# Kernel tuning notes

Hardware: AMD Instinct MI355X
Metric: run time of the kernel (lower is better)

## Reference

```python
import jax, jax.numpy as jnp
import numpy as np

EPS = 1e-6          # VNLinearLeakyReLU eps
NEG_SLOPE = 0.2     # leaky relu slope
K = 16              # k-NN neighbors
F_EPS = 1e-12       # F.normalize eps


def vn_linear_leaky(x, Wf, Wd):
    # x: [B, Cin, 3, ...]; Wf, Wd: [Cout, Cin] (torch nn.Linear, no bias)
    p = jnp.einsum('oc,bc...->bo...', Wf, x)
    d = jnp.einsum('oc,bc...->bo...', Wd, x)
    dot = jnp.sum(p * d, axis=2, keepdims=True)
    d_sq = jnp.sum(d * d, axis=2, keepdims=True)
    mask = (dot >= 0).astype(x.dtype)
    return NEG_SLOPE * p + (1.0 - NEG_SLOPE) * (
        mask * p + (1.0 - mask) * (p - (dot / (d_sq + EPS)) * d))


def channel_equi_vec_normalize(x):
    # x: [B, C, 3, ...]
    norm = jnp.linalg.norm(x, axis=2, keepdims=True)            # [B,C,1,...]
    x_dir = x / jnp.maximum(norm, F_EPS)                        # F.normalize(dim=2)
    ch_norm = jnp.linalg.norm(norm, axis=1, keepdims=True)      # [B,1,1,...]
    x_nn = norm / jnp.maximum(ch_norm, F_EPS)                   # F.normalize(dim=1)
    return x_dir * x_nn


def get_graph_feature(y, k):
    # y: [B, C, 3, N] -> [B, 2C, 3, N, k]  (DGCNN/VN graph feature)
    B, C, _, N = y.shape
    yf = y.reshape(B, C * 3, N)
    sq = jnp.sum(yf * yf, axis=1)                               # [B,N]
    inner = jnp.einsum('bcn,bcm->bnm', yf, yf)
    neg_dist = 2.0 * inner - sq[:, :, None] - sq[:, None, :]    # -||yi-yj||^2
    _, idx = jax.lax.top_k(neg_dist, k)                         # [B,N,k] int32
    yp = jnp.transpose(y, (0, 3, 1, 2))                         # [B,N,C,3]
    nbr = jax.vmap(lambda pts, ids: pts[ids])(yp, idx)          # [B,N,k,C,3]
    center = jnp.broadcast_to(yp[:, :, None], nbr.shape)        # [B,N,k,C,3]
    feat = jnp.concatenate([nbr - center, center], axis=3)      # [B,N,k,2C,3]
    return jnp.transpose(feat, (0, 3, 4, 1, 2))                 # [B,2C,3,N,k]


def setup_inputs() -> dict:
    key = jax.random.key(0)
    ks = jax.random.split(key, 8)
    B, C, N = 2, 32, 768
    x = jax.random.normal(ks[0], (B, C, 3, N), dtype=jnp.float32)
    y = jax.random.normal(ks[1], (B, C, 3, N), dtype=jnp.float32)
    def lin(k, o, i):
        return jax.random.normal(k, (o, i), dtype=jnp.float32) / jnp.sqrt(jnp.float32(i))
    return {
        'x': x, 'y': y,
        'Wq_f': lin(ks[2], 32, 32), 'Wq_d': lin(ks[3], 32, 32),
        'Wk_f': lin(ks[4], 32, 64), 'Wk_d': lin(ks[5], 32, 64),
        'Wv_f': lin(ks[6], 32, 64), 'Wv_d': lin(ks[7], 32, 64),
    }


def reference(x, y, Wq_f, Wq_d, Wk_f, Wk_d, Wv_f, Wv_d):
    Qx = channel_equi_vec_normalize(vn_linear_leaky(x, Wq_f, Wq_d))   # [B,32,3,N]
    g = get_graph_feature(y, K)                                       # [B,64,3,N,K]
    Ky = channel_equi_vec_normalize(vn_linear_leaky(g, Wk_f, Wk_d))   # [B,32,3,N,K]
    Vy = vn_linear_leaky(g, Wv_f, Wv_d)                               # [B,32,3,N,K]
    # Original: Qx repeated over k, matmul([N,k],[k,N]) -> attn[n,m] = Qx[n]*sum_j Ky[m,j]
    scale = 1.0 / jnp.sqrt(jnp.float32(3 * 32))
    Ksum = jnp.sum(Ky, axis=-1)                                       # [B,32,3,N]
    attn = Qx[..., :, None] * Ksum[..., None, :] * scale              # [B,32,3,N,N]
    ax = jax.nn.softmax(attn, axis=-1)
    # sum_k(ax @ Vy) == ax @ sum_k(Vy)
    Vsum = jnp.sum(Vy, axis=-1)                                       # [B,32,3,N]
    out = jnp.einsum('bcdnm,bcdm->bcdn', ax, Vsum)
    return x + out
```

## Files before the change

### kernel.cpp

```cpp
#include <hip/hip_runtime.h>

#define NPTS 768
#define SCALE 0.10206207261596575f

static __device__ const float CFACT[13] = {
  1.0f, 1.0f, 0.5f, 0.16666667f, 0.041666668f, 0.008333334f, 0.0013888889f,
  1.9841270e-4f, 2.4801587e-5f, 2.7557319e-6f, 2.7557319e-7f, 2.5052108e-8f, 2.0876757e-9f
};

__global__ __launch_bounds__(256) void ka_pre(const float* __restrict__ x,
    const float* __restrict__ y,
    const float* __restrict__ Wqf, const float* __restrict__ Wqd,
    const float* __restrict__ Wkf, const float* __restrict__ Wkd,
    const float* __restrict__ Wvf, const float* __restrict__ Wvd,
    float* __restrict__ qx, float* __restrict__ Pb, float* __restrict__ Rb,
    int* __restrict__ idxout)
{
  __shared__ __align__(16) char smem[34816];
  int tid = threadIdx.x;
  if (blockIdx.x < 192) {
    float2* w2 = (float2*)smem;
    float4 (*xs)[32] = (float4(*)[32])(smem + 8192);
    for (int i = tid; i < 1024; i += 256) {
      int cin = i >> 5, c = i & 31;
      w2[i] = make_float2(Wqf[c * 32 + cin], Wqd[c * 32 + cin]);
    }
    int g = tid >> 5, c = tid & 31;
    int p = blockIdx.x * 8 + g;
    int b = p / NPTS, n = p % NPTS;
    for (int t = c; t < 96; t += 32) {
      float v = x[(b * 96 + t) * NPTS + n];
      ((float*)&xs[g][t / 3])[t % 3] = v;
    }
    __syncthreads();
    float pf0 = 0, pf1 = 0, pf2 = 0, pd0 = 0, pd1 = 0, pd2 = 0;
#pragma unroll
    for (int cin = 0; cin < 32; cin++) {
      float2 w = w2[(cin << 5) + c];
      float4 xv = xs[g][cin];
      pf0 = fmaf(w.x, xv.x, pf0); pf1 = fmaf(w.x, xv.y, pf1); pf2 = fmaf(w.x, xv.z, pf2);
      pd0 = fmaf(w.y, xv.x, pd0); pd1 = fmaf(w.y, xv.y, pd1); pd2 = fmaf(w.y, xv.z, pd2);
    }
    float dot = pf0 * pd0 + pf1 * pd1 + pf2 * pd2;
    float dsq = pd0 * pd0 + pd1 * pd1 + pd2 * pd2;
    float q0 = pf0, q1 = pf1, q2 = pf2;
    if (dot < 0.f) {
      float r = 0.8f * dot / (dsq + 1e-6f);
      q0 -= r * pd0; q1 -= r * pd1; q2 -= r * pd2;
    }
    float nrm = sqrtf(q0 * q0 + q1 * q1 + q2 * q2);
    float n2 = nrm * nrm;
#pragma unroll
    for (int m = 1; m <= 16; m <<= 1) n2 += __shfl_xor(n2, m);
    float fac = (nrm / fmaxf(sqrtf(n2), 1e-12f)) / fmaxf(nrm, 1e-12f);
    int base = ((b * 32 + c) * 3) * NPTS + n;
    qx[base] = q0 * fac; qx[base + NPTS] = q1 * fac; qx[base + 2 * NPTS] = q2 * fac;
  } else if (blockIdx.x < 576) {
    float4* wLs = (float4*)smem;
    float4* wDs = (float4*)(smem + 16384);
    float4 (*xs)[32] = (float4(*)[32])(smem + 32768);
    for (int i = tid; i < 1024; i += 256) {
      int cin = i >> 5, c = i & 31;
      float kfL = Wkf[c * 64 + cin], kdL = Wkd[c * 64 + cin];
      float vfL = Wvf[c * 64 + cin], vdL = Wvd[c * 64 + cin];
      wLs[i] = make_float4(kfL, kdL, vfL, vdL);
      wDs[i] = make_float4(Wkf[c * 64 + 32 + cin] - kfL, Wkd[c * 64 + 32 + cin] - kdL,
                           Wvf[c * 64 + 32 + cin] - vfL, Wvd[c * 64 + 32 + cin] - vdL);
    }
    int g = tid >> 6, lane = tid & 63, half = lane >> 5, c = lane & 31;
    int p = (blockIdx.x - 192) * 4 + g;
    int b = p / NPTS, n = p % NPTS;
    for (int t = lane; t < 96; t += 64) {
      float v = y[(b * 96 + t) * NPTS + n];
      ((float*)&xs[g][t / 3])[t % 3] = v;
    }
    __syncthreads();
    const float4* wsel = half ? wDs : wLs;
    float kf0 = 0, kf1 = 0, kf2 = 0, kd0 = 0, kd1 = 0, kd2 = 0;
    float vf0 = 0, vf1 = 0, vf2 = 0, vd0 = 0, vd1 = 0, vd2 = 0;
#pragma unroll 8
    for (int cin = 0; cin < 32; cin++) {
      float4 wv = wsel[(cin << 5) + c];
      float4 xv = xs[g][cin];
      kf0 = fmaf(wv.x, xv.x, kf0); kf1 = fmaf(wv.x, xv.y, kf1); kf2 = fmaf(wv.x, xv.z, kf2);
      kd0 = fmaf(wv.y, xv.x, kd0); kd1 = fmaf(wv.y, xv.y, kd1); kd2 = fmaf(wv.y, xv.z, kd2);
      vf0 = fmaf(wv.z, xv.x, vf0); vf1 = fmaf(wv.z, xv.y, vf1); vf2 = fmaf(wv.z, xv.z, vf2);
      vd0 = fmaf(wv.w, xv.x, vd0); vd1 = fmaf(wv.w, xv.y, vd1); vd2 = fmaf(wv.w, xv.z, vd2);
    }
    float* dst = half ? Rb : Pb;
    size_t base = ((size_t)(b * NPTS + n) * 32 + c) * 12;
    float4* Dp = (float4*)(dst + base);
    Dp[0] = make_float4(kf0, kf1, kf2, kd0);
    Dp[1] = make_float4(kd1, kd2, vf0, vf1);
    Dp[2] = make_float4(vf2, vd0, vd1, vd2);
  } else {
    float4 (*as4)[24] = (float4(*)[24])smem;
    unsigned int (*kd)[NPTS] = (unsigned int(*)[NPTS])(smem + 1536);
    int kb = blockIdx.x - 576;
    int b = kb / 192;
    int n0 = (kb % 192) * 4;
    const float* yb = y + b * 96 * NPTS;
    for (int i = tid; i < 384; i += 256) {
      int j = i / 96, f = i % 96;
      ((float*)as4)[j * 96 + f] = yb[f * NPTS + n0 + j];
    }
    __syncthreads();
    float in[12];
    float sqm[3] = {0.f, 0.f, 0.f};
#pragma unroll
    for (int t = 0; t < 12; t++) in[t] = 0.f;
#pragma unroll 4
    for (int f4 = 0; f4 < 24; f4++) {
      float4 a0 = as4[0][f4], a1 = as4[1][f4], a2 = as4[2][f4], a3 = as4[3][f4];
#pragma unroll
      for (int r = 0; r < 3; r++) {
        int m = r * 256 + tid;
        const float* col = yb + (f4 * 4) * NPTS + m;
        float b0 = col[0], b1 = col[NPTS], b2 = col[2 * NPTS], b3 = col[3 * NPTS];
        sqm[r] = fmaf(b0, b0, fmaf(b1, b1, fmaf(b2, b2, fmaf(b3, b3, sqm[r]))));
        in[0 + r] = fmaf(a0.x, b0, fmaf(a0.y, b1, fmaf(a0.z, b2, fmaf(a0.w, b3, in[0 + r]))));
        in[3 + r] = fmaf(a1.x, b0, fmaf(a1.y, b1, fmaf(a1.z, b2, fmaf(a1.w, b3, in[3 + r]))));
        in[6 + r] = fmaf(a2.x, b0, fmaf(a2.y, b1, fmaf(a2.z, b2, fmaf(a2.w, b3, in[6 + r]))));
        in[9 + r] = fmaf(a3.x, b0, fmaf(a3.y, b1, fmaf(a3.z, b2, fmaf(a3.w, b3, in[9 + r]))));
      }
    }
#pragma unroll
    for (int j = 0; j < 4; j++) {
#pragma unroll
      for (int r = 0; r < 3; r++) {
        int m = r * 256 + tid;
        float v = 2.f * in[j * 3 + r] - sqm[r];
        unsigned int u = __float_as_uint(v);
        u = (u & 0x80000000u) ? ~u : (u | 0x80000000u);
        kd[j][m] = u;
      }
    }
    __syncthreads();
    int w = tid >> 6, lane = tid & 63;
    unsigned long long kk[12];
#pragma unroll
    for (int j = 0; j < 12; j++) {
      int m = lane + 64 * j;
      kk[j] = ((unsigned long long)kd[w][m] << 10) | (unsigned)(1023 - m);
    }
    int outbase = (b * NPTS + n0 + w) * 16;
    for (int it = 0; it < 16; it++) {
      unsigned long long a0 = kk[0] > kk[1] ? kk[0] : kk[1];
      unsigned long long a1 = kk[2] > kk[3] ? kk[2] : kk[3];
      unsigned long long a2 = kk[4] > kk[5] ? kk[4] : kk[5];
      unsigned long long a3 = kk[6] > kk[7] ? kk[6] : kk[7];
      unsigned long long a4 = kk[8] > kk[9] ? kk[8] : kk[9];
      unsigned long long a5 = kk[10] > kk[11] ? kk[10] : kk[11];
      unsigned long long b0 = a0 > a1 ? a0 : a1;
      unsigned long long b1 = a2 > a3 ? a2 : a3;
      unsigned long long b2 = a4 > a5 ? a4 : a5;
      unsigned long long best = b0 > b1 ? b0 : b1;
      best = best > b2 ? best : b2;
#pragma unroll
      for (int off = 1; off <= 32; off <<= 1) {
        unsigned long long o = __shfl_xor(best, off);
        best = o > best ? o : best;
      }
      int wm = 1023 - (int)(best & 1023u);
      if (lane == 0) idxout[outbase + it] = wm;
      int jj = wm >> 6;
      bool me = (lane == (wm & 63));
      switch (jj) {
        case 0:  kk[0]  = me ? 0ull : kk[0];  break;
        case 1:  kk[1]  = me ? 0ull : kk[1];  break;
        case 2:  kk[2]  = me ? 0ull : kk[2];  break;
        case 3:  kk[3]  = me ? 0ull : kk[3];  break;
        case 4:  kk[4]  = me ? 0ull : kk[4];  break;
        case 5:  kk[5]  = me ? 0ull : kk[5];  break;
        case 6:  kk[6]  = me ? 0ull : kk[6];  break;
        case 7:  kk[7]  = me ? 0ull : kk[7];  break;
        case 8:  kk[8]  = me ? 0ull : kk[8];  break;
        case 9:  kk[9]  = me ? 0ull : kk[9];  break;
        case 10: kk[10] = me ? 0ull : kk[10]; break;
        default: kk[11] = me ? 0ull : kk[11]; break;
      }
    }
  }
}

__global__ __launch_bounds__(256) void kb_kv(const float* __restrict__ Pb,
    const float* __restrict__ Rb, const int* __restrict__ idxw,
    float* __restrict__ ksum, float* __restrict__ vsum)
{
  __shared__ float red[2][6][32];
  int tid = threadIdx.x;
  int w = tid >> 6;
  int pt = w >> 1;
  int wh = w & 1;
  int lane = tid & 63, kh = lane >> 5, c = lane & 31;
  int p = blockIdx.x * 2 + pt;
  int b = p / NPTS, n = p % NPTS;
  const float4* Rp = (const float4*)(Rb + ((size_t)(b * NPTS + n) * 32 + c) * 12);
  float4 r0 = Rp[0], r1 = Rp[1], r2 = Rp[2];
  int ibase = (b * NPTS + n) * 16 + wh * 8 + kh * 4;
  int4 ia = *(const int4*)(idxw + ibase);
  int ms[4] = {ia.x, ia.y, ia.z, ia.w};
  float ks0 = 0, ks1 = 0, ks2 = 0, vs0 = 0, vs1 = 0, vs2 = 0;
#pragma unroll
  for (int j = 0; j < 4; j++) {
    const float4* Pp = (const float4*)(Pb + ((size_t)(b * NPTS + ms[j]) * 32 + c) * 12);
    float4 p0 = Pp[0], p1 = Pp[1], p2 = Pp[2];
    float kf0 = p0.x + r0.x, kf1 = p0.y + r0.y, kf2 = p0.z + r0.z;
    float kd0 = p0.w + r0.w, kd1 = p1.x + r1.x, kd2 = p1.y + r1.y;
    float vf0 = p1.z + r1.z, vf1 = p1.w + r1.w, vf2 = p2.x + r2.x;
    float vd0 = p2.y + r2.y, vd1 = p2.z + r2.z, vd2 = p2.w + r2.w;
    float dot = kf0 * kd0 + kf1 * kd1 + kf2 * kd2;
    float dsq = kd0 * kd0 + kd1 * kd1 + kd2 * kd2;
    float k0 = kf0, k1 = kf1, k2 = kf2;
    if (dot < 0.f) { float r = 0.8f * dot / (dsq + 1e-6f); k0 -= r * kd0; k1 -= r * kd1; k2 -= r * kd2; }
    float nrm = sqrtf(k0 * k0 + k1 * k1 + k2 * k2);
    float n2 = nrm * nrm;
#pragma unroll
    for (int mm = 1; mm <= 16; mm <<= 1) n2 += __shfl_xor(n2, mm);
    float fac = (nrm / fmaxf(sqrtf(n2), 1e-12f)) / fmaxf(nrm, 1e-12f);
    ks0 = fmaf(k0, fac, ks0); ks1 = fmaf(k1, fac, ks1); ks2 = fmaf(k2, fac, ks2);
    float dotv = vf0 * vd0 + vf1 * vd1 + vf2 * vd2;
    float dsqv = vd0 * vd0 + vd1 * vd1 + vd2 * vd2;
    float v0 = vf0, v1 = vf1, v2 = vf2;
    if (dotv < 0.f) { float r = 0.8f * dotv / (dsqv + 1e-6f); v0 -= r * vd0; v1 -= r * vd1; v2 -= r * vd2; }
    vs0 += v0; vs1 += v1; vs2 += v2;
  }
  ks0 += __shfl_xor(ks0, 32); ks1 += __shfl_xor(ks1, 32); ks2 += __shfl_xor(ks2, 32);
  vs0 += __shfl_xor(vs0, 32); vs1 += __shfl_xor(vs1, 32); vs2 += __shfl_xor(vs2, 32);
  if (kh == 0 && wh == 1) {
    red[pt][0][c] = ks0; red[pt][1][c] = ks1; red[pt][2][c] = ks2;
    red[pt][3][c] = vs0; red[pt][4][c] = vs1; red[pt][5][c] = vs2;
  }
  __syncthreads();
  if (kh == 0 && wh == 0) {
    ks0 += red[pt][0][c]; ks1 += red[pt][1][c]; ks2 += red[pt][2][c];
    vs0 += red[pt][3][c]; vs1 += red[pt][4][c]; vs2 += red[pt][5][c];
    int base = ((b * 32 + c) * 3) * NPTS + n;
    ksum[base] = ks0 * SCALE; ksum[base + NPTS] = ks1 * SCALE; ksum[base + 2 * NPTS] = ks2 * SCALE;
    vsum[base] = vs0; vsum[base + NPTS] = vs1; vsum[base + 2 * NPTS] = vs2;
  }
}

__global__ __launch_bounds__(256) void kc_attn(const float* __restrict__ x,
    const float* __restrict__ qx, const float* __restrict__ ks, const float* __restrict__ vs,
    float* __restrict__ out)
{
  __shared__ float red[4][25];
  __shared__ float AB[26];
  int tid = threadIdx.x;
  int sl = blockIdx.x;
  const float* srow = ks + sl * NPTS;
  const float* vrow = vs + sl * NPTS;
  float P[12], Q[13];
#pragma unroll
  for (int t = 0; t < 12; t++) P[t] = 0.f;
#pragma unroll
  for (int t = 0; t < 13; t++) Q[t] = 0.f;
  for (int m = tid; m < NPTS; m += 256) {
    float s = srow[m], v = vrow[m];
    Q[0] += v;
    float pw = s;
#pragma unroll
    for (int t = 0; t < 12; t++) {
      P[t] += pw;
      Q[t + 1] = fmaf(pw, v, Q[t + 1]);
      pw *= s;
    }
  }
#pragma unroll
  for (int off = 1; off <= 32; off <<= 1) {
#pragma unroll
    for (int t = 0; t < 12; t++) P[t] += __shfl_xor(P[t], off);
#pragma unroll
    for (int t = 0; t < 13; t++) Q[t] += __shfl_xor(Q[t], off);
  }
  int lane = tid & 63, wid = tid >> 6;
  if (lane == 0) {
#pragma unroll
    for (int t = 0; t < 12; t++) red[wid][t] = P[t];
#pragma unroll
    for (int t = 0; t < 13; t++) red[wid][12 + t] = Q[t];
  }
  __syncthreads();
  if (tid < 25) {
    float sm = red[0][tid] + red[1][tid] + red[2][tid] + red[3][tid];
    if (tid < 12) AB[1 + tid] = CFACT[1 + tid] * sm;
    else          AB[13 + (tid - 12)] = CFACT[tid - 12] * sm;
  }
  if (tid == 25) AB[0] = (float)NPTS;
  __syncthreads();
#pragma unroll
  for (int nn = 0; nn < 3; nn++) {
    int n = nn * 256 + tid;
    float q = qx[sl * NPTS + n];
    float den = AB[12], num = AB[25];
#pragma unroll
    for (int t = 11; t >= 0; t--) {
      den = fmaf(den, q, AB[t]);
      num = fmaf(num, q, AB[13 + t]);
    }
    out[sl * NPTS + n] = x[sl * NPTS + n] + num / den;
  }
}

extern "C" void kernel_launch(void* const* d_in, const int* in_sizes, int n_in,
                              void* d_out, int out_size, void* d_ws, size_t ws_size,
                              hipStream_t stream) {
  const float* x   = (const float*)d_in[0];
  const float* y   = (const float*)d_in[1];
  const float* Wqf = (const float*)d_in[2];
  const float* Wqd = (const float*)d_in[3];
  const float* Wkf = (const float*)d_in[4];
  const float* Wkd = (const float*)d_in[5];
  const float* Wvf = (const float*)d_in[6];
  const float* Wvd = (const float*)d_in[7];
  float* out = (float*)d_out;

  float* qx   = (float*)d_ws;
  float* ksum = qx + 147456;
  float* vsum = ksum + 147456;
  int*   idx  = (int*)(vsum + 147456);
  float* Pb   = (float*)(idx + 24576);
  float* Rb   = Pb + 589824;

  ka_pre <<<960, 256, 0, stream>>>(x, y, Wqf, Wqd, Wkf, Wkd, Wvf, Wvd, qx, Pb, Rb, idx);
  kb_kv  <<<768, 256, 0, stream>>>(Pb, Rb, idx, ksum, vsum);
  kc_attn<<<192, 256, 0, stream>>>(x, qx, ksum, vsum, out);
}
```

Before: 114.5 us.

## Merge Q projection into KV blocks and widen kNN tiles to eight rows

The Q-projection branch is folded into the K/V projection blocks, so each block loads both x and y for its point and the lower half of each wave also computes the normalized Qx. The kNN branch now handles 8 query rows per block instead of 4, which halves the number of times each y column is reread from global memory. Each wave then runs the top-16 selection for two rows in sequence. Grid size drops from 960 to 576 blocks, at the cost of more shared memory, more registers in the distance loop, and longer serial top-k work per block.

New measurement: 123.4 us. 7.7% more time.

```diff
diff --git a/kernel.cpp b/kernel.cpp
--- a/kernel.cpp
+++ b/kernel.cpp
@@ -16,49 +16,14 @@
     float* __restrict__ qx, float* __restrict__ Pb, float* __restrict__ Rb,
     int* __restrict__ idxout)
 {
-  __shared__ __align__(16) char smem[34816];
+  __shared__ __align__(16) char smem[45056];
   int tid = threadIdx.x;
-  if (blockIdx.x < 192) {
-    float2* w2 = (float2*)smem;
-    float4 (*xs)[32] = (float4(*)[32])(smem + 8192);
-    for (int i = tid; i < 1024; i += 256) {
-      int cin = i >> 5, c = i & 31;
-      w2[i] = make_float2(Wqf[c * 32 + cin], Wqd[c * 32 + cin]);
-    }
-    int g = tid >> 5, c = tid & 31;
-    int p = blockIdx.x * 8 + g;
-    int b = p / NPTS, n = p % NPTS;
-    for (int t = c; t < 96; t += 32) {
-      float v = x[(b * 96 + t) * NPTS + n];
-      ((float*)&xs[g][t / 3])[t % 3] = v;
-    }
-    __syncthreads();
-    float pf0 = 0, pf1 = 0, pf2 = 0, pd0 = 0, pd1 = 0, pd2 = 0;
-#pragma unroll
-    for (int cin = 0; cin < 32; cin++) {
-      float2 w = w2[(cin << 5) + c];
-      float4 xv = xs[g][cin];
-      pf0 = fmaf(w.x, xv.x, pf0); pf1 = fmaf(w.x, xv.y, pf1); pf2 = fmaf(w.x, xv.z, pf2);
-      pd0 = fmaf(w.y, xv.x, pd0); pd1 = fmaf(w.y, xv.y, pd1); pd2 = fmaf(w.y, xv.z, pd2);
-    }
-    float dot = pf0 * pd0 + pf1 * pd1 + pf2 * pd2;
-    float dsq = pd0 * pd0 + pd1 * pd1 + pd2 * pd2;
-    float q0 = pf0, q1 = pf1, q2 = pf2;
-    if (dot < 0.f) {
-      float r = 0.8f * dot / (dsq + 1e-6f);
-      q0 -= r * pd0; q1 -= r * pd1; q2 -= r * pd2;
-    }
-    float nrm = sqrtf(q0 * q0 + q1 * q1 + q2 * q2);
-    float n2 = nrm * nrm;
-#pragma unroll
-    for (int m = 1; m <= 16; m <<= 1) n2 += __shfl_xor(n2, m);
-    float fac = (nrm / fmaxf(sqrtf(n2), 1e-12f)) / fmaxf(nrm, 1e-12f);
-    int base = ((b * 32 + c) * 3) * NPTS + n;
-    qx[base] = q0 * fac; qx[base + NPTS] = q1 * fac; qx[base + 2 * NPTS] = q2 * fac;
-  } else if (blockIdx.x < 576) {
+  if (blockIdx.x < 384) {
     float4* wLs = (float4*)smem;
     float4* wDs = (float4*)(smem + 16384);
-    float4 (*xs)[32] = (float4(*)[32])(smem + 32768);
+    float2* wq2 = (float2*)(smem + 32768);
+    float4 (*xs)[32] = (float4(*)[32])(smem + 40960);
+    float4 (*xq)[32] = (float4(*)[32])(smem + 43008);
     for (int i = tid; i < 1024; i += 256) {
       int cin = i >> 5, c = i & 31;
       float kfL = Wkf[c * 64 + cin], kdL = Wkd[c * 64 + cin];
@@ -66,13 +31,14 @@
       wLs[i] = make_float4(kfL, kdL, vfL, vdL);
       wDs[i] = make_float4(Wkf[c * 64 + 32 + cin] - kfL, Wkd[c * 64 + 32 + cin] - kdL,
                            Wvf[c * 64 + 32 + cin] - vfL, Wvd[c * 64 + 32 + cin] - vdL);
+      wq2[i] = make_float2(Wqf[c * 32 + cin], Wqd[c * 32 + cin]);
     }
     int g = tid >> 6, lane = tid & 63, half = lane >> 5, c = lane & 31;
-    int p = (blockIdx.x - 192) * 4 + g;
+    int p = blockIdx.x * 4 + g;
     int b = p / NPTS, n = p % NPTS;
     for (int t = lane; t < 96; t += 64) {
-      float v = y[(b * 96 + t) * NPTS + n];
-      ((float*)&xs[g][t / 3])[t % 3] = v;
+      ((float*)&xs[g][t / 3])[t % 3] = y[(b * 96 + t) * NPTS + n];
+      ((float*)&xq[g][t / 3])[t % 3] = x[(b * 96 + t) * NPTS + n];
     }
     __syncthreads();
     const float4* wsel = half ? wDs : wLs;
@@ -93,39 +59,68 @@
     Dp[0] = make_float4(kf0, kf1, kf2, kd0);
     Dp[1] = make_float4(kd1, kd2, vf0, vf1);
     Dp[2] = make_float4(vf2, vd0, vd1, vd2);
+    if (half == 0) {
+      float pf0 = 0, pf1 = 0, pf2 = 0, pd0 = 0, pd1 = 0, pd2 = 0;
+#pragma unroll 8
+      for (int cin = 0; cin < 32; cin++) {
+        float2 w = wq2[(cin << 5) + c];
+        float4 xv = xq[g][cin];
+        pf0 = fmaf(w.x, xv.x, pf0); pf1 = fmaf(w.x, xv.y, pf1); pf2 = fmaf(w.x, xv.z, pf2);
+        pd0 = fmaf(w.y, xv.x, pd0); pd1 = fmaf(w.y, xv.y, pd1); pd2 = fmaf(w.y, xv.z, pd2);
+      }
+      float dot = pf0 * pd0 + pf1 * pd1 + pf2 * pd2;
+      float dsq = pd0 * pd0 + pd1 * pd1 + pd2 * pd2;
+      float q0 = pf0, q1 = pf1, q2 = pf2;
+      if (dot < 0.f) {
+        float r = 0.8f * dot / (dsq + 1e-6f);
+        q0 -= r * pd0; q1 -= r * pd1; q2 -= r * pd2;
+      }
+      float nrm = sqrtf(q0 * q0 + q1 * q1 + q2 * q2);
+      float n2 = nrm * nrm;
+#pragma unroll
+      for (int m = 1; m <= 16; m <<= 1) n2 += __shfl_xor(n2, m);
+      float fac = (nrm / fmaxf(sqrtf(n2), 1e-12f)) / fmaxf(nrm, 1e-12f);
+      int qb = ((b * 32 + c) * 3) * NPTS + n;
+      qx[qb] = q0 * fac; qx[qb + NPTS] = q1 * fac; qx[qb + 2 * NPTS] = q2 * fac;
+    }
   } else {
     float4 (*as4)[24] = (float4(*)[24])smem;
-    unsigned int (*kd)[NPTS] = (unsigned int(*)[NPTS])(smem + 1536);
-    int kb = blockIdx.x - 576;
-    int b = kb / 192;
-    int n0 = (kb % 192) * 4;
+    unsigned int (*kd)[NPTS] = (unsigned int(*)[NPTS])(smem + 3072);
+    int kbn = blockIdx.x - 384;
+    int b = kbn / 96;
+    int n0 = (kbn % 96) * 8;
     const float* yb = y + b * 96 * NPTS;
-    for (int i = tid; i < 384; i += 256) {
+    for (int i = tid; i < 768; i += 256) {
       int j = i / 96, f = i % 96;
       ((float*)as4)[j * 96 + f] = yb[f * NPTS + n0 + j];
     }
     __syncthreads();
-    float in[12];
+    float in[24];
     float sqm[3] = {0.f, 0.f, 0.f};
 #pragma unroll
-    for (int t = 0; t < 12; t++) in[t] = 0.f;
-#pragma unroll 4
+    for (int t = 0; t < 24; t++) in[t] = 0.f;
+#pragma unroll 2
     for (int f4 = 0; f4 < 24; f4++) {
       float4 a0 = as4[0][f4], a1 = as4[1][f4], a2 = as4[2][f4], a3 = as4[3][f4];
+      float4 a4 = as4[4][f4], a5 = as4[5][f4], a6 = as4[6][f4], a7 = as4[7][f4];
 #pragma unroll
       for (int r = 0; r < 3; r++) {
         int m = r * 256 + tid;
         const float* col = yb + (f4 * 4) * NPTS + m;
         float b0 = col[0], b1 = col[NPTS], b2 = col[2 * NPTS], b3 = col[3 * NPTS];
         sqm[r] = fmaf(b0, b0, fmaf(b1, b1, fmaf(b2, b2, fmaf(b3, b3, sqm[r]))));
-        in[0 + r] = fmaf(a0.x, b0, fmaf(a0.y, b1, fmaf(a0.z, b2, fmaf(a0.w, b3, in[0 + r]))));
-        in[3 + r] = fmaf(a1.x, b0, fmaf(a1.y, b1, fmaf(a1.z, b2, fmaf(a1.w, b3, in[3 + r]))));
-        in[6 + r] = fmaf(a2.x, b0, fmaf(a2.y, b1, fmaf(a2.z, b2, fmaf(a2.w, b3, in[6 + r]))));
-        in[9 + r] = fmaf(a3.x, b0, fmaf(a3.y, b1, fmaf(a3.z, b2, fmaf(a3.w, b3, in[9 + r]))));
-      }
-    }
-#pragma unroll
-    for (int j = 0; j < 4; j++) {
+        in[0 + r]  = fmaf(a0.x, b0, fmaf(a0.y, b1, fmaf(a0.z, b2, fmaf(a0.w, b3, in[0 + r]))));
+        in[3 + r]  = fmaf(a1.x, b0, fmaf(a1.y, b1, fmaf(a1.z, b2, fmaf(a1.w, b3, in[3 + r]))));
+        in[6 + r]  = fmaf(a2.x, b0, fmaf(a2.y, b1, fmaf(a2.z, b2, fmaf(a2.w, b3, in[6 + r]))));
+        in[9 + r]  = fmaf(a3.x, b0, fmaf(a3.y, b1, fmaf(a3.z, b2, fmaf(a3.w, b3, in[9 + r]))));
+        in[12 + r] = fmaf(a4.x, b0, fmaf(a4.y, b1, fmaf(a4.z, b2, fmaf(a4.w, b3, in[12 + r]))));
+        in[15 + r] = fmaf(a5.x, b0, fmaf(a5.y, b1, fmaf(a5.z, b2, fmaf(a5.w, b3, in[15 + r]))));
+        in[18 + r] = fmaf(a6.x, b0, fmaf(a6.y, b1, fmaf(a6.z, b2, fmaf(a6.w, b3, in[18 + r]))));
+        in[21 + r] = fmaf(a7.x, b0, fmaf(a7.y, b1, fmaf(a7.z, b2, fmaf(a7.w, b3, in[21 + r]))));
+      }
+    }
+#pragma unroll
+    for (int j = 0; j < 8; j++) {
 #pragma unroll
       for (int r = 0; r < 3; r++) {
         int m = r * 256 + tid;
@@ -137,47 +132,50 @@
     }
     __syncthreads();
     int w = tid >> 6, lane = tid & 63;
-    unsigned long long kk[12];
-#pragma unroll
-    for (int j = 0; j < 12; j++) {
-      int m = lane + 64 * j;
-      kk[j] = ((unsigned long long)kd[w][m] << 10) | (unsigned)(1023 - m);
-    }
-    int outbase = (b * NPTS + n0 + w) * 16;
-    for (int it = 0; it < 16; it++) {
-      unsigned long long a0 = kk[0] > kk[1] ? kk[0] : kk[1];
-      unsigned long long a1 = kk[2] > kk[3] ? kk[2] : kk[3];
-      unsigned long long a2 = kk[4] > kk[5] ? kk[4] : kk[5];
-      unsigned long long a3 = kk[6] > kk[7] ? kk[6] : kk[7];
-      unsigned long long a4 = kk[8] > kk[9] ? kk[8] : kk[9];
-      unsigned long long a5 = kk[10] > kk[11] ? kk[10] : kk[11];
-      unsigned long long b0 = a0 > a1 ? a0 : a1;
-      unsigned long long b1 = a2 > a3 ? a2 : a3;
-      unsigned long long b2 = a4 > a5 ? a4 : a5;
-      unsigned long long best = b0 > b1 ? b0 : b1;
-      best = best > b2 ? best : b2;
-#pragma unroll
-      for (int off = 1; off <= 32; off <<= 1) {
-        unsigned long long o = __shfl_xor(best, off);
-        best = o > best ? o : best;
-      }
-      int wm = 1023 - (int)(best & 1023u);
-      if (lane == 0) idxout[outbase + it] = wm;
-      int jj = wm >> 6;
-      bool me = (lane == (wm & 63));
-      switch (jj) {
-        case 0:  kk[0]  = me ? 0ull : kk[0];  break;
-        case 1:  kk[1]  = me ? 0ull : kk[1];  break;
-        case 2:  kk[2]  = me ? 0ull : kk[2];  break;
-        case 3:  kk[3]  = me ? 0ull : kk[3];  break;
-        case 4:  kk[4]  = me ? 0ull : kk[4];  break;
-        case 5:  kk[5]  = me ? 0ull : kk[5];  break;
-        case 6:  kk[6]  = me ? 0ull : kk[6];  break;
-        case 7:  kk[7]  = me ? 0ull : kk[7];  break;
-        case 8:  kk[8]  = me ? 0ull : kk[8];  break;
-        case 9:  kk[9]  = me ? 0ull : kk[9];  break;
-        case 10: kk[10] = me ? 0ull : kk[10]; break;
-        default: kk[11] = me ? 0ull : kk[11]; break;
+    for (int rr = 0; rr < 2; rr++) {
+      int row = w + rr * 4;
+      unsigned long long kk[12];
+#pragma unroll
+      for (int j = 0; j < 12; j++) {
+        int m = lane + 64 * j;
+        kk[j] = ((unsigned long long)kd[row][m] << 10) | (unsigned)(1023 - m);
+      }
+      int outbase = (b * NPTS + n0 + row) * 16;
+      for (int it = 0; it < 16; it++) {
+        unsigned long long a0 = kk[0] > kk[1] ? kk[0] : kk[1];
+        unsigned long long a1 = kk[2] > kk[3] ? kk[2] : kk[3];
+        unsigned long long a2 = kk[4] > kk[5] ? kk[4] : kk[5];
+        unsigned long long a3 = kk[6] > kk[7] ? kk[6] : kk[7];
+        unsigned long long a4 = kk[8] > kk[9] ? kk[8] : kk[9];
+        unsigned long long a5 = kk[10] > kk[11] ? kk[10] : kk[11];
+        unsigned long long b0 = a0 > a1 ? a0 : a1;
+        unsigned long long b1 = a2 > a3 ? a2 : a3;
+        unsigned long long b2 = a4 > a5 ? a4 : a5;
+        unsigned long long best = b0 > b1 ? b0 : b1;
+        best = best > b2 ? best : b2;
+#pragma unroll
+        for (int off = 1; off <= 32; off <<= 1) {
+          unsigned long long o = __shfl_xor(best, off);
+          best = o > best ? o : best;
+        }
+        int wm = 1023 - (int)(best & 1023u);
+        if (lane == 0) idxout[outbase + it] = wm;
+        int jj = wm >> 6;
+        bool me = (lane == (wm & 63));
+        switch (jj) {
+          case 0:  kk[0]  = me ? 0ull : kk[0];  break;
+          case 1:  kk[1]  = me ? 0ull : kk[1];  break;
+          case 2:  kk[2]  = me ? 0ull : kk[2];  break;
+          case 3:  kk[3]  = me ? 0ull : kk[3];  break;
+          case 4:  kk[4]  = me ? 0ull : kk[4];  break;
+          case 5:  kk[5]  = me ? 0ull : kk[5];  break;
+          case 6:  kk[6]  = me ? 0ull : kk[6];  break;
+          case 7:  kk[7]  = me ? 0ull : kk[7];  break;
+          case 8:  kk[8]  = me ? 0ull : kk[8];  break;
+          case 9:  kk[9]  = me ? 0ull : kk[9];  break;
+          case 10: kk[10] = me ? 0ull : kk[10]; break;
+          default: kk[11] = me ? 0ull : kk[11]; break;
+        }
       }
     }
   }
@@ -323,7 +321,7 @@
   float* Pb   = (float*)(idx + 24576);
   float* Rb   = Pb + 589824;
 
-  ka_pre <<<960, 256, 0, stream>>>(x, y, Wqf, Wqd, Wkf, Wkd, Wvf, Wvd, qx, Pb, Rb, idx);
+  ka_pre <<<576, 256, 0, stream>>>(x, y, Wqf, Wqd, Wkf, Wkd, Wvf, Wvd, qx, Pb, Rb, idx);
   kb_kv  <<<768, 256, 0, stream>>>(Pb, Rb, idx, ksum, vsum);
   kc_attn<<<192, 256, 0, stream>>>(x, qx, ksum, vsum, out);
 }
```
